# Optimization experiments

Hardware: AMD Instinct MI355X
Metric: run time of the kernel (lower is better)

Reference implementation:

```python
import jax, jax.numpy as jnp
import numpy as np
from jax import lax

BN_EPS = 1e-5


def conv(x, w, b, pad):
    # x: NCHW, w: OIHW
    y = lax.conv_general_dilated(x, w, (1, 1), [(pad, pad), (pad, pad)],
                                 dimension_numbers=('NCHW', 'OIHW', 'NCHW'))
    return y + b[None, :, None, None]


def conv_t(x, w, b):
    # ConvTranspose2d, stride=1, padding=0, kernel 3. w is torch layout [in, out, kh, kw].
    # Equivalent to a regular conv with spatially flipped kernel, in/out swapped, full padding (kh-1=2).
    wf = jnp.transpose(jnp.flip(w, (2, 3)), (1, 0, 2, 3))  # [out, in, kh, kw]
    y = lax.conv_general_dilated(x, wf, (1, 1), [(2, 2), (2, 2)],
                                 dimension_numbers=('NCHW', 'OIHW', 'NCHW'))
    return y + b[None, :, None, None]


def bn(x, g, be):
    # BatchNorm2d, training-mode batch stats (biased variance), gamma/beta learnable.
    mu = x.mean((0, 2, 3), keepdims=True)
    var = x.var((0, 2, 3), keepdims=True)
    xn = (x - mu) * lax.rsqrt(var + BN_EPS)
    return g[None, :, None, None] * xn + be[None, :, None, None]


def setup_inputs() -> dict:
    key = jax.random.key(0)
    ks = jax.random.split(key, 20)
    B, C, H, W = 16, 64, 44, 44
    P = H * W  # 1936

    def kaiming(k, shape, fan_out):
        return jax.random.normal(k, shape, jnp.float32) * np.sqrt(2.0 / fan_out)

    inp = {
        'depth': jax.random.normal(ks[0], (B, C, H, W), jnp.float32),
        'rgb': jax.random.normal(ks[1], (B, C, H, W), jnp.float32),
        # h_c / h_f conv layers: Conv2d(128, 64, 3, padding=1)
        'w_hc': kaiming(ks[2], (64, 128, 3, 3), 64 * 9), 'b_hc': jnp.zeros((64,), jnp.float32),
        'w_hf': kaiming(ks[3], (64, 128, 3, 3), 64 * 9), 'b_hf': jnp.zeros((64,), jnp.float32),
        # spatial_pool_agr
        'w_s1': kaiming(ks[4], (32, P, 3, 3), 32 * 9), 'bs1': jnp.zeros((32,), jnp.float32),
        'g1': jnp.ones((32,), jnp.float32), 'be1': jnp.zeros((32,), jnp.float32),
        'w_s2': kaiming(ks[5], (32, 32, 3, 3), 32 * 9), 'bs2': jnp.zeros((32,), jnp.float32),
        'g2': jnp.ones((32,), jnp.float32), 'be2': jnp.zeros((32,), jnp.float32),
        # ConvTranspose2d weights in torch layout [in, out, kh, kw]
        'w_d1': kaiming(ks[6], (32, 32, 3, 3), 32 * 9), 'bd1': jnp.zeros((32,), jnp.float32),
        'g3': jnp.ones((32,), jnp.float32), 'be3': jnp.zeros((32,), jnp.float32),
        'w_d2': kaiming(ks[7], (32, 1, 3, 3), 1 * 9), 'bd2': jnp.zeros((1,), jnp.float32),
        # channel_pool_ag: Linear(64, 16), Linear(16, 64)
        'w_l1': kaiming(ks[8], (16, 64), 16), 'bl1': jnp.zeros((16,), jnp.float32),
        'w_l2': kaiming(ks[9], (64, 16), 64), 'bl2': jnp.zeros((64,), jnp.float32),
    }
    return inp


def reference(depth, rgb, w_hc, b_hc, w_hf, b_hf,
              w_s1, bs1, g1, be1, w_s2, bs2, g2, be2,
              w_d1, bd1, g3, be3, w_d2, bd2,
              w_l1, bl1, w_l2, bl2):
    B, C, H, W = depth.shape
    # fused rgb+depth conv
    h_c = jnp.concatenate([rgb, depth], axis=1)          # [B, 2C, H, W]
    h_c_conv = jax.nn.relu(conv(h_c, w_hc, b_hc, 1))      # [B, 64, H, W]

    # per-pixel correlation: grouped 1x1 conv == batched matmul
    # pixel_corr[b, p, y, x] = sum_c rgb[b, c, y, x] * depth[b, c, p]
    pixel_corr = jnp.einsum('bchw,bcp->bphw', rgb, depth.reshape(B, C, H * W))

    x = jax.nn.relu(bn(conv(pixel_corr, w_s1, bs1, 0), g1, be1))  # 44 -> 42
    x = jax.nn.relu(bn(conv(x, w_s2, bs2, 0), g2, be2))           # 42 -> 40
    x = jax.nn.relu(bn(conv_t(x, w_d1, bd1), g3, be3))            # 40 -> 42
    spatial_att = jax.nn.sigmoid(conv_t(x, w_d2, bd2))            # [B, 1, 44, 44]

    # per-channel correlation: grouped full-extent conv == elementwise dot per (b, c)
    depth_corr = jnp.sum(rgb * depth, axis=(2, 3))                # [B, C]
    # MaxPool2d(1)/AvgPool2d(1) are identities -> both branches are identical
    def mlp(v):
        return jax.nn.relu(v @ w_l1.T + bl1) @ w_l2.T + bl2
    m = mlp(depth_corr)
    channel_att = jax.nn.sigmoid(m + m)[:, :, None, None]         # [B, C, 1, 1]

    h_att = jnp.concatenate([h_c_conv * spatial_att, h_c_conv * channel_att], axis=1)
    return jax.nn.relu(conv(h_att, w_hf, b_hf, 1))                # [B, 64, 44, 44]
```

## Files before the change

kernel.cpp:

```cpp
#include <hip/hip_runtime.h>
#include <math.h>

#define P_ 1936
#define EPS_ 1e-5f

typedef __attribute__((ext_vector_type(8))) short bf16x8;
typedef __attribute__((ext_vector_type(4))) float f32x4;
typedef __attribute__((ext_vector_type(4))) ushort u16x4;

__device__ __forceinline__ ushort f2bf(float f) {
    union { float f; unsigned u; } v; v.f = f;
    unsigned u = v.u;
    return (ushort)((u + 0x7FFFu + ((u >> 16) & 1u)) >> 16);
}
__device__ __forceinline__ float bf2f(ushort h) {
    union { unsigned u; float f; } v; v.u = (unsigned)h << 16;
    return v.f;
}

__device__ __forceinline__ void bn_coef(const float* stats, const float* g,
                                        const float* be, int ch, float inv_n,
                                        float& sc, float& sh) {
    float sum = stats[ch*2], sq = stats[ch*2+1];
    float mu = sum * inv_n;
    float var = sq * inv_n - mu*mu;
    float r = rsqrtf(var + EPS_);
    sc = g[ch] * r;
    sh = be[ch] - mu * sc;
}

__global__ __launch_bounds__(256) void k_setup(const float* __restrict__ whc,
                                               const float* __restrict__ whf,
                                               const float* __restrict__ ws2,
                                               const float* __restrict__ wd1,
                                               const float* __restrict__ ws1,
                                               const float* __restrict__ rgb,
                                               const float* __restrict__ depth,
                                               ushort* __restrict__ wpck,
                                               ushort* __restrict__ a2,
                                               ushort* __restrict__ a3,
                                               ushort* __restrict__ apck1,
                                               ushort* __restrict__ xp,
                                               ushort* __restrict__ depthb,
                                               float* __restrict__ dcor,
                                               float* __restrict__ stats) {
    __shared__ float r8[8];
    const int bx = blockIdx.x, t = threadIdx.x;
    if (bx < 2808) {
        if (bx == 0 && t < 192) stats[t] = 0.f;
        int idx = bx * 256 + t;
        if (idx < 147456) {
            const float* src = (idx < 73728) ? whc : whf;
            int j = (idx < 73728) ? idx : idx - 73728;
            int kk = j / 8192, rem = j - kk * 8192;
            int o = rem >> 7, c = rem & 127;
            wpck[(idx < 73728 ? 0 : 73728) + (kk * 64 + o) * 128 + c] =
                f2bf(src[(size_t)(o * 128 + c) * 9 + kk]);
        } else if (idx < 156672) {
            int j = idx - 147456;
            int kk = j >> 10, rem = j & 1023, o = rem >> 5, c = rem & 31;
            a2[j] = f2bf(ws2[((size_t)o*32 + c)*9 + kk]);
            a3[j] = f2bf(wd1[((size_t)c*32 + o)*9 + (8 - kk)]);
        } else if (idx < 718848) {
            int j = idx - 156672;
            int m = j / 1952, p = j - m*1952;
            int o = m / 9, kk = m - o*9;
            apck1[j] = (p < P_) ? f2bf(ws1[((size_t)o*P_ + p)*9 + kk]) : (ushort)0;
        }
        return;
    }
    const int j = bx - 2808;
    const int g8 = j & 7, b = j >> 3;
    const int c0 = g8 * 8;
    const float* rsrc = rgb   + ((size_t)b*64 + c0)*P_;
    const float* dsrc = depth + ((size_t)b*64 + c0)*P_;
    ushort* xr = xp + ((size_t)(b*16 + g8))*2300*8;
    ushort* xd = xp + ((size_t)(b*16 + 8 + g8))*2300*8;
    if (t < 8) r8[t] = 0.f;
    __syncthreads();
    float dc[8];
    #pragma unroll
    for (int e = 0; e < 8; ++e) dc[e] = 0.f;

    for (int pos = t; pos < 2300; pos += 256) {
        int y1 = pos / 50, x1 = pos - y1*50;
        uint4 vr = {0u,0u,0u,0u}, vd = {0u,0u,0u,0u};
        if (y1 >= 1 && y1 <= 44 && x1 >= 1 && x1 <= 44) {
            int p = (y1-1)*44 + (x1-1);
            ushort hr[8], hd[8];
            #pragma unroll
            for (int e = 0; e < 8; ++e) {
                float fr = rsrc[(size_t)e*P_ + p];
                float fd = dsrc[(size_t)e*P_ + p];
                dc[e] = fmaf(fr, fd, dc[e]);
                hr[e] = f2bf(fr); hd[e] = f2bf(fd);
            }
            vr.x = hr[0] | ((unsigned)hr[1] << 16); vr.y = hr[2] | ((unsigned)hr[3] << 16);
            vr.z = hr[4] | ((unsigned)hr[5] << 16); vr.w = hr[6] | ((unsigned)hr[7] << 16);
            vd.x = hd[0] | ((unsigned)hd[1] << 16); vd.y = hd[2] | ((unsigned)hd[3] << 16);
            vd.z = hd[4] | ((unsigned)hd[5] << 16); vd.w = hd[6] | ((unsigned)hd[7] << 16);
        }
        *(uint4*)(xr + (size_t)pos*8) = vr;
        *(uint4*)(xd + (size_t)pos*8) = vd;
    }
    for (int idx = t; idx < 8*488; idx += 256) {
        int e = idx / 488, jj = idx - e*488;
        u16x4 h = {0,0,0,0};
        if (jj < 484) {
            float4 f4 = *(const float4*)(dsrc + (size_t)e*P_ + jj*4);
            h[0] = f2bf(f4.x); h[1] = f2bf(f4.y); h[2] = f2bf(f4.z); h[3] = f2bf(f4.w);
        }
        *(u16x4*)(depthb + ((size_t)(b*64 + c0 + e))*1952 + jj*4) = h;
    }
    #pragma unroll
    for (int e = 0; e < 8; ++e) {
        float v = dc[e];
        #pragma unroll
        for (int off = 32; off > 0; off >>= 1) v += __shfl_down(v, off, 64);
        if ((t & 63) == 0) atomicAdd(&r8[e], v);
    }
    __syncthreads();
    if (t < 8) dcor[b*64 + c0 + t] = r8[t];
}

__global__ __launch_bounds__(256) void k_hcconv(const ushort* __restrict__ xp,
                                                const ushort* __restrict__ wt,
                                                const float* __restrict__ bias,
                                                ushort* __restrict__ hcp) {
    __shared__ ushort lds[9616];
    const int rt = blockIdx.x, og = blockIdx.y, b = blockIdx.z, t = threadIdx.x;
    const int w = t >> 6, lane = t & 63, lr = lane & 15, lg = lane >> 4;
    const int r0 = rt * 4;
    f32x4 acc[2][3];
    #pragma unroll
    for (int mf = 0; mf < 2; ++mf)
        #pragma unroll
        for (int nf = 0; nf < 3; ++nf)
            acc[mf][nf] = (f32x4){0.f, 0.f, 0.f, 0.f};

    for (int s = 0; s < 4; ++s) {
        __syncthreads();
        const ushort* gsrc = xp + ((size_t)(b*16 + s*4))*2300*8;
        for (int u = t; u < 1200; u += 256) {
            int cg = u / 300, rem = u - cg*300;
            int rr = rem / 50, xx = rem - rr*50;
            uint4 v = *(const uint4*)(gsrc + (((size_t)cg*46 + (r0+rr))*50 + xx)*8);
            *(uint4*)(lds + (size_t)u*8) = v;
        }
        __syncthreads();
        const int abase = s*32 + lg*8;
        #pragma unroll
        for (int kk = 0; kk < 9; ++kk) {
            bf16x8 af[2];
            #pragma unroll
            for (int mf = 0; mf < 2; ++mf)
                af[mf] = *(const bf16x8*)(wt + (size_t)(kk*64 + og*32 + mf*16 + lr)*128 + abase);
            const int ky = kk / 3, kx = kk - ky*3;
            #pragma unroll
            for (int nf = 0; nf < 3; ++nf) {
                bf16x8 bf = *(const bf16x8*)&lds[((lg*6 + (w + ky))*50 + (nf*16 + lr + kx))*8];
                #pragma unroll
                for (int mf = 0; mf < 2; ++mf)
                    acc[mf][nf] = __builtin_amdgcn_mfma_f32_16x16x32_bf16(af[mf], bf, acc[mf][nf], 0, 0, 0);
            }
        }
    }
    const int y = r0 + w;
    #pragma unroll
    for (int nf = 0; nf < 3; ++nf) {
        int x = nf*16 + lr;
        if (x < 44) {
            #pragma unroll
            for (int mf = 0; mf < 2; ++mf) {
                u16x4 pk;
                #pragma unroll
                for (int i = 0; i < 4; ++i) {
                    int ol = mf*16 + lg*4 + i;
                    pk[i] = f2bf(fmaxf(acc[mf][nf][i] + bias[og*32 + ol], 0.f));
                }
                int g = og*4 + mf*2 + (lg >> 1);
                *(u16x4*)(hcp + (((size_t)(b*8 + g)*46 + (y+1))*50 + (x+1))*8 + (lg&1)*4) = pk;
            }
        }
    }
}

__global__ __launch_bounds__(256) void k_final(const ushort* __restrict__ hcp,
                                               const float* __restrict__ satt,
                                               const float* __restrict__ catt,
                                               const ushort* __restrict__ wt,
                                               const float* __restrict__ bias,
                                               float* __restrict__ out) {
    __shared__ ushort lds[9616];
    __shared__ float catv[64];
    const int rt = blockIdx.x, og = blockIdx.y, b = blockIdx.z, t = threadIdx.x;
    const int w = t >> 6, lane = t & 63, lr = lane & 15, lg = lane >> 4;
    const int r0 = rt * 4;
    if (t < 64) catv[t] = catt[b*64 + t];
    f32x4 acc[2][3];
    #pragma unroll
    for (int mf = 0; mf < 2; ++mf)
        #pragma unroll
        for (int nf = 0; nf < 3; ++nf)
            acc[mf][nf] = (f32x4){0.f, 0.f, 0.f, 0.f};

    for (int s = 0; s < 4; ++s) {
        __syncthreads();
        for (int u = t; u < 1200; u += 256) {
            int cg = u / 300, rem = u - cg*300;
            int rr = rem / 50, xx = rem - rr*50;
            int g = s*4 + cg;
            int y1 = r0 + rr;
            uint4 v = {0u,0u,0u,0u};
            if (y1 >= 1 && y1 <= 44 && xx >= 1 && xx <= 44) {
                int gs = (g < 8) ? g : (g - 8);
                uint4 raw = *(const uint4*)(hcp + (((size_t)(b*8 + gs)*46 + y1)*50 + xx)*8);
                unsigned arr[4] = {raw.x, raw.y, raw.z, raw.w};
                ushort h[8];
                if (g < 8) {
                    float att = satt[(size_t)b*P_ + (y1-1)*44 + (xx-1)];
                    #pragma unroll
                    for (int e = 0; e < 8; ++e) {
                        ushort hv = (e & 1) ? (ushort)(arr[e>>1] >> 16) : (ushort)(arr[e>>1] & 0xffffu);
                        h[e] = f2bf(bf2f(hv) * att);
                    }
                } else {
                    #pragma unroll
                    for (int e = 0; e < 8; ++e) {
                        ushort hv = (e & 1) ? (ushort)(arr[e>>1] >> 16) : (ushort)(arr[e>>1] & 0xffffu);
                        h[e] = f2bf(bf2f(hv) * catv[(g-8)*8 + e]);
                    }
                }
                v.x = h[0] | ((unsigned)h[1] << 16);
                v.y = h[2] | ((unsigned)h[3] << 16);
                v.z = h[4] | ((unsigned)h[5] << 16);
                v.w = h[6] | ((unsigned)h[7] << 16);
            }
            *(uint4*)(lds + (size_t)u*8) = v;
        }
        __syncthreads();
        const int abase = s*32 + lg*8;
        #pragma unroll
        for (int kk = 0; kk < 9; ++kk) {
            bf16x8 af[2];
            #pragma unroll
            for (int mf = 0; mf < 2; ++mf)
                af[mf] = *(const bf16x8*)(wt + (size_t)(kk*64 + og*32 + mf*16 + lr)*128 + abase);
            const int ky = kk / 3, kx = kk - ky*3;
            #pragma unroll
            for (int nf = 0; nf < 3; ++nf) {
                bf16x8 bf = *(const bf16x8*)&lds[((lg*6 + (w + ky))*50 + (nf*16 + lr + kx))*8];
                #pragma unroll
                for (int mf = 0; mf < 2; ++mf)
                    acc[mf][nf] = __builtin_amdgcn_mfma_f32_16x16x32_bf16(af[mf], bf, acc[mf][nf], 0, 0, 0);
            }
        }
    }
    const int y = r0 + w;
    #pragma unroll
    for (int nf = 0; nf < 3; ++nf) {
        int x = nf*16 + lr;
        if (x < 44) {
            #pragma unroll
            for (int mf = 0; mf < 2; ++mf) {
                #pragma unroll
                for (int i = 0; i < 4; ++i) {
                    int o = og*32 + mf*16 + lg*4 + i;
                    out[(((size_t)b*64 + o)*44 + y)*44 + x] = fmaxf(acc[mf][nf][i] + bias[o], 0.f);
                }
            }
        }
    }
}

__global__ __launch_bounds__(256) void k_Umfma(const ushort* __restrict__ apck1,
                                               const ushort* __restrict__ depthb,
                                               ushort* __restrict__ upck,
                                               const float* __restrict__ dcorr,
                                               const float* __restrict__ wl1,
                                               const float* __restrict__ bl1,
                                               const float* __restrict__ wl2,
                                               const float* __restrict__ bl2,
                                               float* __restrict__ catt) {
    const int mt = blockIdx.x, b = blockIdx.y, t = threadIdx.x;
    if (mt == 18) {
        __shared__ float dc[64], h[16];
        if (t < 64) dc[t] = dcorr[b*64 + t];
        __syncthreads();
        if (t < 16) {
            float a = bl1[t];
            #pragma unroll 8
            for (int c = 0; c < 64; ++c) a = fmaf(dc[c], wl1[t*64 + c], a);
            h[t] = fmaxf(a, 0.f);
        }
        __syncthreads();
        if (t < 64) {
            float m = bl2[t];
            #pragma unroll
            for (int jj = 0; jj < 16; ++jj) m = fmaf(h[jj], wl2[t*16 + jj], m);
            catt[b*64 + t] = 1.f / (1.f + expf(-2.f*m));
        }
        return;
    }
    const int nt = t >> 6, lane = t & 63, lr = lane & 15, lg = lane >> 4;
    f32x4 acc = (f32x4){0.f, 0.f, 0.f, 0.f};
    const ushort* ap = apck1 + (size_t)(mt*16 + lr)*1952 + lg*8;
    const ushort* bp = depthb + ((size_t)(b*64) + nt*16 + lr)*1952 + lg*8;
    #pragma unroll 4
    for (int ks = 0; ks < 61; ++ks) {
        bf16x8 af = *(const bf16x8*)(ap + ks*32);
        bf16x8 bf = *(const bf16x8*)(bp + ks*32);
        acc = __builtin_amdgcn_mfma_f32_16x16x32_bf16(af, bf, acc, 0, 0, 0);
    }
    #pragma unroll
    for (int i = 0; i < 4; ++i) {
        int m = mt*16 + lg*4 + i;
        int o = m / 9, kk = m - o*9;
        upck[((size_t)(b*9 + kk)*32 + o)*64 + nt*16 + lr] = f2bf(acc[i]);
    }
}

__global__ __launch_bounds__(256) void k_conv1_mfma(const ushort* __restrict__ xp,
                                                    const ushort* __restrict__ upck,
                                                    const float* __restrict__ bs1,
                                                    ushort* __restrict__ z1p,
                                                    float* __restrict__ stats) {
    __shared__ ushort lds[8*6*50*8 + 32];
    __shared__ float ssum[32], ssq[32];
    const int rt = blockIdx.x, b = blockIdx.y, t = threadIdx.x;
    const int w = t >> 6, lane = t & 63, lr = lane & 15, lg = lane >> 4;
    const int r0 = rt * 4;
    if (t < 32) { ssum[t] = 0.f; ssq[t] = 0.f; }
    f32x4 acc[2][3];
    #pragma unroll
    for (int mf = 0; mf < 2; ++mf)
        #pragma unroll
        for (int nf = 0; nf < 3; ++nf)
            acc[mf][nf] = (f32x4){0.f, 0.f, 0.f, 0.f};

    const ushort* gsrc = xp + (size_t)b*16*2300*8;
    for (int u = t; u < 2400; u += 256) {
        int cg = u / 300, rem = u - cg*300;
        int rr = rem / 50, xx = rem - rr*50;
        int y1 = min(r0 + 1 + rr, 45);
        *(uint4*)(lds + (size_t)u*8) = *(const uint4*)(gsrc + (((size_t)cg*46 + y1)*50 + xx)*8);
    }
    __syncthreads();
    #pragma unroll
    for (int s = 0; s < 2; ++s) {
        #pragma unroll
        for (int kk = 0; kk < 9; ++kk) {
            bf16x8 af[2];
            #pragma unroll
            for (int mf = 0; mf < 2; ++mf)
                af[mf] = *(const bf16x8*)(upck + ((size_t)(b*9 + kk)*32 + mf*16 + lr)*64 + s*32 + lg*8);
            const int ky = kk / 3, kx = kk - ky*3;
            #pragma unroll
            for (int nf = 0; nf < 3; ++nf) {
                bf16x8 bv = *(const bf16x8*)&lds[(((s*4 + lg)*6 + (w + ky))*50 + (nf*16 + lr + kx + 1))*8];
                #pragma unroll
                for (int mf = 0; mf < 2; ++mf)
                    acc[mf][nf] = __builtin_amdgcn_mfma_f32_16x16x32_bf16(af[mf], bv, acc[mf][nf], 0, 0, 0);
            }
        }
    }
    const int y = r0 + w;
    const int cb = lg*4;
    if (y < 42) {
        float ls[2][4], lq[2][4], br[2][4];
        #pragma unroll
        for (int mf = 0; mf < 2; ++mf)
            #pragma unroll
            for (int i = 0; i < 4; ++i) {
                ls[mf][i] = 0.f; lq[mf][i] = 0.f;
                br[mf][i] = bs1[mf*16 + cb + i];
            }
        #pragma unroll
        for (int nf = 0; nf < 3; ++nf) {
            int x = nf*16 + lr;
            bool xv = (x < 42);
            #pragma unroll
            for (int mf = 0; mf < 2; ++mf) {
                u16x4 pk;
                #pragma unroll
                for (int i = 0; i < 4; ++i) {
                    float v = acc[mf][nf][i] + br[mf][i];
                    if (xv) { ls[mf][i] += v; lq[mf][i] = fmaf(v, v, lq[mf][i]); }
                    pk[i] = f2bf(v);
                }
                if (xv) {
                    int cg1 = mf*2 + (lg >> 1);
                    *(u16x4*)(z1p + ((((size_t)b*4 + cg1)*42 + y)*48 + x)*8 + (lg&1)*4) = pk;
                }
            }
        }
        #pragma unroll
        for (int mf = 0; mf < 2; ++mf)
            #pragma unroll
            for (int i = 0; i < 4; ++i) {
                float s0 = ls[mf][i], q0 = lq[mf][i];
                #pragma unroll
                for (int m = 1; m < 16; m <<= 1) { s0 += __shfl_xor(s0, m, 64); q0 += __shfl_xor(q0, m, 64); }
                if (lr == 0) { atomicAdd(&ssum[mf*16 + cb + i], s0); atomicAdd(&ssq[mf*16 + cb + i], q0); }
            }
    }
    __syncthreads();
    if (t < 32) { atomicAdd(&stats[t*2], ssum[t]); atomicAdd(&stats[t*2+1], ssq[t]); }
}

__global__ __launch_bounds__(256) void k_conv2_mfma(const ushort* __restrict__ z1p,
                                                    const ushort* __restrict__ apck,
                                                    const float* __restrict__ bs2,
                                                    const float* __restrict__ g1,
                                                    const float* __restrict__ be1,
                                                    const float* __restrict__ statsIn,
                                                    ushort* __restrict__ z2p,
                                                    float* __restrict__ statsOut) {
    __shared__ ushort lds[4*6*48*8 + 32];
    __shared__ float sc[32], sh[32], ssum[32], ssq[32];
    const int rt = blockIdx.x, b = blockIdx.y, t = threadIdx.x;
    const int w = t >> 6, lane = t & 63, lr = lane & 15, lg = lane >> 4;
    const int r0 = rt * 4;
    if (t < 32) {
        bn_coef(statsIn, g1, be1, t, 1.f/28224.f, sc[t], sh[t]);
        ssum[t] = 0.f; ssq[t] = 0.f;
    }
    __syncthreads();
    f32x4 acc[2][3];
    #pragma unroll
    for (int mf = 0; mf < 2; ++mf)
        #pragma unroll
        for (int nf = 0; nf < 3; ++nf)
            acc[mf][nf] = (f32x4){0.f, 0.f, 0.f, 0.f};

    for (int u = t; u < 1152; u += 256) {
        int cg = u / 288, rem = u - cg*288;
        int rr = rem / 48, xx = rem - rr*48;
        uint4 raw = *(const uint4*)(z1p + ((((size_t)b*4 + cg)*42 + (r0 + rr))*48 + xx)*8);
        unsigned arr[4] = {raw.x, raw.y, raw.z, raw.w};
        ushort h[8];
        #pragma unroll
        for (int e = 0; e < 8; ++e) {
            ushort hv = (e & 1) ? (ushort)(arr[e>>1] >> 16) : (ushort)(arr[e>>1] & 0xffffu);
            float f = fmaxf(fmaf(bf2f(hv), sc[cg*8 + e], sh[cg*8 + e]), 0.f);
            h[e] = f2bf(f);
        }
        uint4 v;
        v.x = h[0] | ((unsigned)h[1] << 16);
        v.y = h[2] | ((unsigned)h[3] << 16);
        v.z = h[4] | ((unsigned)h[5] << 16);
        v.w = h[6] | ((unsigned)h[7] << 16);
        *(uint4*)(lds + (size_t)u*8) = v;
    }
    __syncthreads();
    #pragma unroll
    for (int kk = 0; kk < 9; ++kk) {
        bf16x8 af[2];
        #pragma unroll
        for (int mf = 0; mf < 2; ++mf)
            af[mf] = *(const bf16x8*)(apck + (size_t)(kk*32 + mf*16 + lr)*32 + lg*8);
        const int ky = kk / 3, kx = kk - ky*3;
        #pragma unroll
        for (int nf = 0; nf < 3; ++nf) {
            bf16x8 bv = *(const bf16x8*)&lds[((lg*6 + (w + ky))*48 + (nf*16 + lr + kx))*8];
            #pragma unroll
            for (int mf = 0; mf < 2; ++mf)
                acc[mf][nf] = __builtin_amdgcn_mfma_f32_16x16x32_bf16(af[mf], bv, acc[mf][nf], 0, 0, 0);
        }
    }
    const int y = r0 + w;
    const int cb = lg*4;
    {
        float ls[2][4], lq[2][4], br[2][4];
        #pragma unroll
        for (int mf = 0; mf < 2; ++mf)
            #pragma unroll
            for (int i = 0; i < 4; ++i) {
                ls[mf][i] = 0.f; lq[mf][i] = 0.f;
                br[mf][i] = bs2[mf*16 + cb + i];
            }
        #pragma unroll
        for (int nf = 0; nf < 3; ++nf) {
            int x = nf*16 + lr;
            bool xv = (x < 40);
            #pragma unroll
            for (int mf = 0; mf < 2; ++mf) {
                u16x4 pk;
                #pragma unroll
                for (int i = 0; i < 4; ++i) {
                    float v = acc[mf][nf][i] + br[mf][i];
                    if (xv) { ls[mf][i] += v; lq[mf][i] = fmaf(v, v, lq[mf][i]); }
                    pk[i] = f2bf(v);
                }
                if (xv) {
                    int cg1 = mf*2 + (lg >> 1);
                    *(u16x4*)(z2p + ((((size_t)b*4 + cg1)*46 + (y+2))*48 + (x+2))*8 + (lg&1)*4) = pk;
                }
            }
        }
        #pragma unroll
        for (int mf = 0; mf < 2; ++mf)
            #pragma unroll
            for (int i = 0; i < 4; ++i) {
                float s0 = ls[mf][i], q0 = lq[mf][i];
                #pragma unroll
                for (int m = 1; m < 16; m <<= 1) { s0 += __shfl_xor(s0, m, 64); q0 += __shfl_xor(q0, m, 64); }
                if (lr == 0) { atomicAdd(&ssum[mf*16 + cb + i], s0); atomicAdd(&ssq[mf*16 + cb + i], q0); }
            }
    }
    __syncthreads();
    if (t < 32) { atomicAdd(&statsOut[t*2], ssum[t]); atomicAdd(&statsOut[t*2+1], ssq[t]); }
}

__global__ __launch_bounds__(256) void k_dconv1_mfma(const ushort* __restrict__ z2p,
                                                     const ushort* __restrict__ apck,
                                                     const float* __restrict__ bd1,
                                                     const float* __restrict__ g2,
                                                     const float* __restrict__ be2,
                                                     const float* __restrict__ statsIn,
                                                     ushort* __restrict__ z3p,
                                                     float* __restrict__ statsOut) {
    __shared__ ushort lds[4*6*48*8 + 32];
    __shared__ float sc[32], sh[32], ssum[32], ssq[32];
    const int rt = blockIdx.x, b = blockIdx.y, t = threadIdx.x;
    const int w = t >> 6, lane = t & 63, lr = lane & 15, lg = lane >> 4;
    const int r0 = rt * 4;
    if (t < 32) {
        bn_coef(statsIn, g2, be2, t, 1.f/25600.f, sc[t], sh[t]);
        ssum[t] = 0.f; ssq[t] = 0.f;
    }
    __syncthreads();
    f32x4 acc[2][3];
    #pragma unroll
    for (int mf = 0; mf < 2; ++mf)
        #pragma unroll
        for (int nf = 0; nf < 3; ++nf)
            acc[mf][nf] = (f32x4){0.f, 0.f, 0.f, 0.f};

    for (int u = t; u < 1152; u += 256) {
        int cg = u / 288, rem = u - cg*288;
        int rr = rem / 48, xx = rem - rr*48;
        int row = r0 + rr;
        uint4 v = {0u,0u,0u,0u};
        if (row >= 2 && row <= 41 && xx >= 2 && xx <= 41) {
            uint4 raw = *(const uint4*)(z2p + ((((size_t)b*4 + cg)*46 + row)*48 + xx)*8);
            unsigned arr[4] = {raw.x, raw.y, raw.z, raw.w};
            ushort h[8];
            #pragma unroll
            for (int e = 0; e < 8; ++e) {
                ushort hv = (e & 1) ? (ushort)(arr[e>>1] >> 16) : (ushort)(arr[e>>1] & 0xffffu);
                float f = fmaxf(fmaf(bf2f(hv), sc[cg*8 + e], sh[cg*8 + e]), 0.f);
                h[e] = f2bf(f);
            }
            v.x = h[0] | ((unsigned)h[1] << 16);
            v.y = h[2] | ((unsigned)h[3] << 16);
            v.z = h[4] | ((unsigned)h[5] << 16);
            v.w = h[6] | ((unsigned)h[7] << 16);
        }
        *(uint4*)(lds + (size_t)u*8) = v;
    }
    __syncthreads();
    #pragma unroll
    for (int kk = 0; kk < 9; ++kk) {
        bf16x8 af[2];
        #pragma unroll
        for (int mf = 0; mf < 2; ++mf)
            af[mf] = *(const bf16x8*)(apck + (size_t)(kk*32 + mf*16 + lr)*32 + lg*8);
        const int ky = kk / 3, kx = kk - ky*3;
        #pragma unroll
        for (int nf = 0; nf < 3; ++nf) {
            bf16x8 bv = *(const bf16x8*)&lds[((lg*6 + (w + ky))*48 + (nf*16 + lr + kx))*8];
            #pragma unroll
            for (int mf = 0; mf < 2; ++mf)
                acc[mf][nf] = __builtin_amdgcn_mfma_f32_16x16x32_bf16(af[mf], bv, acc[mf][nf], 0, 0, 0);
        }
    }
    const int y = r0 + w;
    const int cb = lg*4;
    if (y < 42) {
        float ls[2][4], lq[2][4], br[2][4];
        #pragma unroll
        for (int mf = 0; mf < 2; ++mf)
            #pragma unroll
            for (int i = 0; i < 4; ++i) {
                ls[mf][i] = 0.f; lq[mf][i] = 0.f;
                br[mf][i] = bd1[mf*16 + cb + i];
            }
        #pragma unroll
        for (int nf = 0; nf < 3; ++nf) {
            int x = nf*16 + lr;
            bool xv = (x < 42);
            #pragma unroll
            for (int mf = 0; mf < 2; ++mf) {
                u16x4 pk;
                #pragma unroll
                for (int i = 0; i < 4; ++i) {
                    float v = acc[mf][nf][i] + br[mf][i];
                    if (xv) { ls[mf][i] += v; lq[mf][i] = fmaf(v, v, lq[mf][i]); }
                    pk[i] = f2bf(v);
                }
                if (xv) {
                    int cg1 = mf*2 + (lg >> 1);
                    *(u16x4*)(z3p + ((((size_t)b*4 + cg1)*46 + (y+2))*48 + (x+2))*8 + (lg&1)*4) = pk;
                }
            }
        }
        #pragma unroll
        for (int mf = 0; mf < 2; ++mf)
            #pragma unroll
            for (int i = 0; i < 4; ++i) {
                float s0 = ls[mf][i], q0 = lq[mf][i];
                #pragma unroll
                for (int m = 1; m < 16; m <<= 1) { s0 += __shfl_xor(s0, m, 64); q0 += __shfl_xor(q0, m, 64); }
                if (lr == 0) { atomicAdd(&ssum[mf*16 + cb + i], s0); atomicAdd(&ssq[mf*16 + cb + i], q0); }
            }
    }
    __syncthreads();
    if (t < 32) { atomicAdd(&statsOut[t*2], ssum[t]); atomicAdd(&statsOut[t*2+1], ssq[t]); }
}

__global__ __launch_bounds__(256) void k_dconv2(const ushort* __restrict__ z3p,
                                                const float* __restrict__ wd2,
                                                const float* __restrict__ bd2,
                                                const float* __restrict__ g3,
                                                const float* __restrict__ be3,
                                                const float* __restrict__ stats,
                                                float* __restrict__ satt) {
    __shared__ float sc[32], sh[32], wf[32][9];
    const int b = blockIdx.y, t = threadIdx.x;
    if (t < 32) bn_coef(stats, g3, be3, t, 1.f/28224.f, sc[t], sh[t]);
    for (int u = t; u < 288; u += 256) {
        int c = u / 9, k = u - c*9;
        wf[c][k] = wd2[c*9 + 8 - k];
    }
    __syncthreads();
    const int pix = blockIdx.x * 256 + t;
    if (pix >= P_) return;
    const int y = pix / 44, x = pix - y*44;
    float acc = bd2[0];
    #pragma unroll
    for (int kk = 0; kk < 9; ++kk) {
        int ky = kk / 3, kx = kk - ky*3;
        int ry = y + ky, rx = x + kx;
        if (ry < 2 || ry > 43 || rx < 2 || rx > 43) continue;
        #pragma unroll
        for (int cg = 0; cg < 4; ++cg) {
            uint4 raw = *(const uint4*)(z3p + ((((size_t)b*4 + cg)*46 + ry)*48 + rx)*8);
            unsigned arr[4] = {raw.x, raw.y, raw.z, raw.w};
            #pragma unroll
            for (int e = 0; e < 8; ++e) {
                ushort hv = (e & 1) ? (ushort)(arr[e>>1] >> 16) : (ushort)(arr[e>>1] & 0xffffu);
                float f = fmaxf(fmaf(bf2f(hv), sc[cg*8 + e], sh[cg*8 + e]), 0.f);
                acc = fmaf(f, wf[cg*8 + e][kk], acc);
            }
        }
    }
    satt[(size_t)b*P_ + pix] = 1.f / (1.f + expf(-acc));
}

extern "C" void kernel_launch(void* const* d_in, const int* in_sizes, int n_in,
                              void* d_out, int out_size, void* d_ws, size_t ws_size,
                              hipStream_t stream) {
    const float* depth = (const float*)d_in[0];
    const float* rgb   = (const float*)d_in[1];
    const float* w_hc  = (const float*)d_in[2];
    const float* b_hc  = (const float*)d_in[3];
    const float* w_hf  = (const float*)d_in[4];
    const float* b_hf  = (const float*)d_in[5];
    const float* w_s1  = (const float*)d_in[6];
    const float* bs1   = (const float*)d_in[7];
    const float* g1    = (const float*)d_in[8];
    const float* be1   = (const float*)d_in[9];
    const float* w_s2  = (const float*)d_in[10];
    const float* bs2   = (const float*)d_in[11];
    const float* g2    = (const float*)d_in[12];
    const float* be2   = (const float*)d_in[13];
    const float* w_d1  = (const float*)d_in[14];
    const float* bd1   = (const float*)d_in[15];
    const float* g3    = (const float*)d_in[16];
    const float* be3   = (const float*)d_in[17];
    const float* w_d2  = (const float*)d_in[18];
    const float* bd2   = (const float*)d_in[19];
    const float* w_l1  = (const float*)d_in[20];
    const float* bl1   = (const float*)d_in[21];
    const float* w_l2  = (const float*)d_in[22];
    const float* bl2   = (const float*)d_in[23];

    float* out = (float*)d_out;
    float* ws  = (float*)d_ws;

    float* satt  = ws;
    float* catt  = satt + 30976;
    float* dcor  = catt + 1024;
    float* stats = dcor + 1024;
    ushort* hcp    = (ushort*)(stats + 192);
    ushort* wpck   = hcp    + 2355200;
    ushort* apck2  = wpck   + 147456;
    ushort* apck3  = apck2  + 9216;
    ushort* apck1  = apck3  + 9216;
    ushort* depthb = apck1  + 562176;
    ushort* upck   = depthb + 1998848;
    ushort* z1p    = upck   + 294912;
    ushort* z2p    = z1p    + 1032192;
    ushort* z3p    = z2p    + 1130496;
    ushort* xpck   = z3p    + 1130496;

    k_setup<<<2936, 256, 0, stream>>>(w_hc, w_hf, w_s2, w_d1, w_s1, rgb, depth,
                                      wpck, apck2, apck3, apck1, xpck, depthb, dcor, stats);

    k_hcconv<<<dim3(11,2,16), 256, 0, stream>>>(xpck, wpck, b_hc, hcp);
    k_Umfma<<<dim3(19,16), 256, 0, stream>>>(apck1, depthb, upck,
                                             dcor, w_l1, bl1, w_l2, bl2, catt);

    k_conv1_mfma<<<dim3(11,16), 256, 0, stream>>>(xpck, upck, bs1, z1p, stats);
    k_conv2_mfma<<<dim3(10,16), 256, 0, stream>>>(z1p, apck2, bs2, g1, be1, stats, z2p, stats + 64);
    k_dconv1_mfma<<<dim3(11,16), 256, 0, stream>>>(z2p, apck3, bd1, g2, be2, stats + 64, z3p, stats + 128);
    k_dconv2<<<dim3(8,16), 256, 0, stream>>>(z3p, w_d2, bd2, g3, be3, stats + 128, satt);

    k_final<<<dim3(11,2,16), 256, 0, stream>>>(hcp, satt, catt, wpck + 73728, b_hf, out);
}
```

Measured before the change: 156.4 us.

## Split setup input-packing blocks 4x and merge hc-conv with U-matmul kernel

The rgb/depth packing part of the setup kernel is split into four position chunks per (batch, channel-group), so it runs as 512 blocks instead of 128. The per-channel dot products are written as four partials that the MLP block sums. The hc conv and the U matmul/MLP kernels are merged into one launch of 656 blocks, which removes a launch and lets the two independent kernels fill the GPU together. The cost is more, smaller blocks and an extra partial-sum buffer.

```diff
diff --git a/kernel.cpp b/kernel.cpp
--- a/kernel.cpp
+++ b/kernel.cpp
@@ -42,7 +42,7 @@
                                                ushort* __restrict__ apck1,
                                                ushort* __restrict__ xp,
                                                ushort* __restrict__ depthb,
-                                               float* __restrict__ dcor,
+                                               float* __restrict__ dcor_part,
                                                float* __restrict__ stats) {
     __shared__ float r8[8];
     const int bx = blockIdx.x, t = threadIdx.x;
@@ -70,7 +70,7 @@
         return;
     }
     const int j = bx - 2808;
-    const int g8 = j & 7, b = j >> 3;
+    const int g8 = j & 7, b = (j >> 3) & 15, q = j >> 7;
     const int c0 = g8 * 8;
     const float* rsrc = rgb   + ((size_t)b*64 + c0)*P_;
     const float* dsrc = depth + ((size_t)b*64 + c0)*P_;
@@ -82,7 +82,8 @@
     #pragma unroll
     for (int e = 0; e < 8; ++e) dc[e] = 0.f;
 
-    for (int pos = t; pos < 2300; pos += 256) {
+    const int pbase = q * 575;
+    for (int pos = pbase + t; pos < pbase + 575; pos += 256) {
         int y1 = pos / 50, x1 = pos - y1*50;
         uint4 vr = {0u,0u,0u,0u}, vd = {0u,0u,0u,0u};
         if (y1 >= 1 && y1 <= 44 && x1 >= 1 && x1 <= 44) {
@@ -103,7 +104,7 @@
         *(uint4*)(xr + (size_t)pos*8) = vr;
         *(uint4*)(xd + (size_t)pos*8) = vd;
     }
-    for (int idx = t; idx < 8*488; idx += 256) {
+    for (int idx = q*976 + t; idx < q*976 + 976; idx += 256) {
         int e = idx / 488, jj = idx - e*488;
         u16x4 h = {0,0,0,0};
         if (jj < 484) {
@@ -120,17 +121,135 @@
         if ((t & 63) == 0) atomicAdd(&r8[e], v);
     }
     __syncthreads();
-    if (t < 8) dcor[b*64 + c0 + t] = r8[t];
-}
-
-__global__ __launch_bounds__(256) void k_hcconv(const ushort* __restrict__ xp,
-                                                const ushort* __restrict__ wt,
-                                                const float* __restrict__ bias,
-                                                ushort* __restrict__ hcp) {
+    if (t < 8) dcor_part[q*1024 + b*64 + c0 + t] = r8[t];
+}
+
+__global__ __launch_bounds__(256) void k_front(const ushort* __restrict__ xp,
+                                               const ushort* __restrict__ wt,
+                                               const float* __restrict__ bhc,
+                                               ushort* __restrict__ hcp,
+                                               const ushort* __restrict__ apck1,
+                                               const ushort* __restrict__ depthb,
+                                               ushort* __restrict__ upck,
+                                               const float* __restrict__ dcor_part,
+                                               const float* __restrict__ wl1,
+                                               const float* __restrict__ bl1,
+                                               const float* __restrict__ wl2,
+                                               const float* __restrict__ bl2,
+                                               float* __restrict__ catt) {
     __shared__ ushort lds[9616];
-    const int rt = blockIdx.x, og = blockIdx.y, b = blockIdx.z, t = threadIdx.x;
+    __shared__ float mlpb[80];
+    const int bx = blockIdx.x, t = threadIdx.x;
+    if (bx < 352) {
+        const int rt = bx % 11, og = (bx / 11) & 1, b = bx / 22;
+        const int w = t >> 6, lane = t & 63, lr = lane & 15, lg = lane >> 4;
+        const int r0 = rt * 4;
+        f32x4 acc[2][3];
+        #pragma unroll
+        for (int mf = 0; mf < 2; ++mf)
+            #pragma unroll
+            for (int nf = 0; nf < 3; ++nf)
+                acc[mf][nf] = (f32x4){0.f, 0.f, 0.f, 0.f};
+
+        for (int s = 0; s < 4; ++s) {
+            __syncthreads();
+            const ushort* gsrc = xp + ((size_t)(b*16 + s*4))*2300*8;
+            for (int u = t; u < 1200; u += 256) {
+                int cg = u / 300, rem = u - cg*300;
+                int rr = rem / 50, xx = rem - rr*50;
+                uint4 v = *(const uint4*)(gsrc + (((size_t)cg*46 + (r0+rr))*50 + xx)*8);
+                *(uint4*)(lds + (size_t)u*8) = v;
+            }
+            __syncthreads();
+            const int abase = s*32 + lg*8;
+            #pragma unroll
+            for (int kk = 0; kk < 9; ++kk) {
+                bf16x8 af[2];
+                #pragma unroll
+                for (int mf = 0; mf < 2; ++mf)
+                    af[mf] = *(const bf16x8*)(wt + (size_t)(kk*64 + og*32 + mf*16 + lr)*128 + abase);
+                const int ky = kk / 3, kx = kk - ky*3;
+                #pragma unroll
+                for (int nf = 0; nf < 3; ++nf) {
+                    bf16x8 bf = *(const bf16x8*)&lds[((lg*6 + (w + ky))*50 + (nf*16 + lr + kx))*8];
+                    #pragma unroll
+                    for (int mf = 0; mf < 2; ++mf)
+                        acc[mf][nf] = __builtin_amdgcn_mfma_f32_16x16x32_bf16(af[mf], bf, acc[mf][nf], 0, 0, 0);
+                }
+            }
+        }
+        const int y = r0 + w;
+        #pragma unroll
+        for (int nf = 0; nf < 3; ++nf) {
+            int x = nf*16 + lr;
+            if (x < 44) {
+                #pragma unroll
+                for (int mf = 0; mf < 2; ++mf) {
+                    u16x4 pk;
+                    #pragma unroll
+                    for (int i = 0; i < 4; ++i) {
+                        int ol = og*32 + mf*16 + lg*4 + i;
+                        pk[i] = f2bf(fmaxf(acc[mf][nf][i] + bhc[ol], 0.f));
+                    }
+                    int g = og*4 + mf*2 + (lg >> 1);
+                    *(u16x4*)(hcp + (((size_t)(b*8 + g)*46 + (y+1))*50 + (x+1))*8 + (lg&1)*4) = pk;
+                }
+            }
+        }
+        return;
+    }
+    const int j = bx - 352;
+    const int mt = j % 19, b = j / 19;
+    if (mt == 18) {
+        float* dcs = mlpb;
+        float* h   = mlpb + 64;
+        if (t < 64) dcs[t] = dcor_part[b*64 + t] + dcor_part[1024 + b*64 + t]
+                           + dcor_part[2048 + b*64 + t] + dcor_part[3072 + b*64 + t];
+        __syncthreads();
+        if (t < 16) {
+            float a = bl1[t];
+            #pragma unroll 8
+            for (int c = 0; c < 64; ++c) a = fmaf(dcs[c], wl1[t*64 + c], a);
+            h[t] = fmaxf(a, 0.f);
+        }
+        __syncthreads();
+        if (t < 64) {
+            float m = bl2[t];
+            #pragma unroll
+            for (int jj = 0; jj < 16; ++jj) m = fmaf(h[jj], wl2[t*16 + jj], m);
+            catt[b*64 + t] = 1.f / (1.f + expf(-2.f*m));
+        }
+        return;
+    }
+    const int nt = t >> 6, lane = t & 63, lr = lane & 15, lg = lane >> 4;
+    f32x4 acc = (f32x4){0.f, 0.f, 0.f, 0.f};
+    const ushort* ap = apck1 + (size_t)(mt*16 + lr)*1952 + lg*8;
+    const ushort* bp = depthb + ((size_t)(b*64) + nt*16 + lr)*1952 + lg*8;
+    #pragma unroll 4
+    for (int ks = 0; ks < 61; ++ks) {
+        bf16x8 af = *(const bf16x8*)(ap + ks*32);
+        bf16x8 bf = *(const bf16x8*)(bp + ks*32);
+        acc = __builtin_amdgcn_mfma_f32_16x16x32_bf16(af, bf, acc, 0, 0, 0);
+    }
+    #pragma unroll
+    for (int i = 0; i < 4; ++i) {
+        int m = mt*16 + lg*4 + i;
+        int o = m / 9, kk = m - o*9;
+        upck[((size_t)(b*9 + kk)*32 + o)*64 + nt*16 + lr] = f2bf(acc[i]);
+    }
+}
+
+__global__ __launch_bounds__(256) void k_conv1_mfma(const ushort* __restrict__ xp,
+                                                    const ushort* __restrict__ upck,
+                                                    const float* __restrict__ bs1,
+                                                    ushort* __restrict__ z1p,
+                                                    float* __restrict__ stats) {
+    __shared__ ushort lds[8*6*50*8 + 32];
+    __shared__ float ssum[32], ssq[32];
+    const int rt = blockIdx.x, b = blockIdx.y, t = threadIdx.x;
     const int w = t >> 6, lane = t & 63, lr = lane & 15, lg = lane >> 4;
     const int r0 = rt * 4;
+    if (t < 32) { ssum[t] = 0.f; ssq[t] = 0.f; }
     f32x4 acc[2][3];
     #pragma unroll
     for (int mf = 0; mf < 2; ++mf)
@@ -138,51 +257,324 @@
         for (int nf = 0; nf < 3; ++nf)
             acc[mf][nf] = (f32x4){0.f, 0.f, 0.f, 0.f};
 
-    for (int s = 0; s < 4; ++s) {
-        __syncthreads();
-        const ushort* gsrc = xp + ((size_t)(b*16 + s*4))*2300*8;
-        for (int u = t; u < 1200; u += 256) {
-            int cg = u / 300, rem = u - cg*300;
-            int rr = rem / 50, xx = rem - rr*50;
-            uint4 v = *(const uint4*)(gsrc + (((size_t)cg*46 + (r0+rr))*50 + xx)*8);
-            *(uint4*)(lds + (size_t)u*8) = v;
-        }
-        __syncthreads();
-        const int abase = s*32 + lg*8;
+    const ushort* gsrc = xp + (size_t)b*16*2300*8;
+    for (int u = t; u < 2400; u += 256) {
+        int cg = u / 300, rem = u - cg*300;
+        int rr = rem / 50, xx = rem - rr*50;
+        int y1 = min(r0 + 1 + rr, 45);
+        *(uint4*)(lds + (size_t)u*8) = *(const uint4*)(gsrc + (((size_t)cg*46 + y1)*50 + xx)*8);
+    }
+    __syncthreads();
+    #pragma unroll
+    for (int s = 0; s < 2; ++s) {
         #pragma unroll
         for (int kk = 0; kk < 9; ++kk) {
             bf16x8 af[2];
             #pragma unroll
             for (int mf = 0; mf < 2; ++mf)
-                af[mf] = *(const bf16x8*)(wt + (size_t)(kk*64 + og*32 + mf*16 + lr)*128 + abase);
+                af[mf] = *(const bf16x8*)(upck + ((size_t)(b*9 + kk)*32 + mf*16 + lr)*64 + s*32 + lg*8);
             const int ky = kk / 3, kx = kk - ky*3;
             #pragma unroll
             for (int nf = 0; nf < 3; ++nf) {
-                bf16x8 bf = *(const bf16x8*)&lds[((lg*6 + (w + ky))*50 + (nf*16 + lr + kx))*8];
+                bf16x8 bv = *(const bf16x8*)&lds[(((s*4 + lg)*6 + (w + ky))*50 + (nf*16 + lr + kx + 1))*8];
                 #pragma unroll
                 for (int mf = 0; mf < 2; ++mf)
-                    acc[mf][nf] = __builtin_amdgcn_mfma_f32_16x16x32_bf16(af[mf], bf, acc[mf][nf], 0, 0, 0);
+                    acc[mf][nf] = __builtin_amdgcn_mfma_f32_16x16x32_bf16(af[mf], bv, acc[mf][nf], 0, 0, 0);
             }
         }
     }
     const int y = r0 + w;
-    #pragma unroll
-    for (int nf = 0; nf < 3; ++nf) {
-        int x = nf*16 + lr;
-        if (x < 44) {
+    const int cb = lg*4;
+    if (y < 42) {
+        float ls[2][4], lq[2][4], br[2][4];
+        #pragma unroll
+        for (int mf = 0; mf < 2; ++mf)
+            #pragma unroll
+            for (int i = 0; i < 4; ++i) {
+                ls[mf][i] = 0.f; lq[mf][i] = 0.f;
+                br[mf][i] = bs1[mf*16 + cb + i];
+            }
+        #pragma unroll
+        for (int nf = 0; nf < 3; ++nf) {
+            int x = nf*16 + lr;
+            bool xv = (x < 42);
             #pragma unroll
             for (int mf = 0; mf < 2; ++mf) {
                 u16x4 pk;
                 #pragma unroll
                 for (int i = 0; i < 4; ++i) {
-                    int ol = mf*16 + lg*4 + i;
-                    pk[i] = f2bf(fmaxf(acc[mf][nf][i] + bias[og*32 + ol], 0.f));
-                }
-                int g = og*4 + mf*2 + (lg >> 1);
-                *(u16x4*)(hcp + (((size_t)(b*8 + g)*46 + (y+1))*50 + (x+1))*8 + (lg&1)*4) = pk;
-            }
-        }
-    }
+                    float v = acc[mf][nf][i] + br[mf][i];
+                    if (xv) { ls[mf][i] += v; lq[mf][i] = fmaf(v, v, lq[mf][i]); }
+                    pk[i] = f2bf(v);
+                }
+                if (xv) {
+                    int cg1 = mf*2 + (lg >> 1);
+                    *(u16x4*)(z1p + ((((size_t)b*4 + cg1)*42 + y)*48 + x)*8 + (lg&1)*4) = pk;
+                }
+            }
+        }
+        #pragma unroll
+        for (int mf = 0; mf < 2; ++mf)
+            #pragma unroll
+            for (int i = 0; i < 4; ++i) {
+                float s0 = ls[mf][i], q0 = lq[mf][i];
+                #pragma unroll
+                for (int m = 1; m < 16; m <<= 1) { s0 += __shfl_xor(s0, m, 64); q0 += __shfl_xor(q0, m, 64); }
+                if (lr == 0) { atomicAdd(&ssum[mf*16 + cb + i], s0); atomicAdd(&ssq[mf*16 + cb + i], q0); }
+            }
+    }
+    __syncthreads();
+    if (t < 32) { atomicAdd(&stats[t*2], ssum[t]); atomicAdd(&stats[t*2+1], ssq[t]); }
+}
+
+__global__ __launch_bounds__(256) void k_conv2_mfma(const ushort* __restrict__ z1p,
+                                                    const ushort* __restrict__ apck,
+                                                    const float* __restrict__ bs2,
+                                                    const float* __restrict__ g1,
+                                                    const float* __restrict__ be1,
+                                                    const float* __restrict__ statsIn,
+                                                    ushort* __restrict__ z2p,
+                                                    float* __restrict__ statsOut) {
+    __shared__ ushort lds[4*6*48*8 + 32];
+    __shared__ float sc[32], sh[32], ssum[32], ssq[32];
+    const int rt = blockIdx.x, b = blockIdx.y, t = threadIdx.x;
+    const int w = t >> 6, lane = t & 63, lr = lane & 15, lg = lane >> 4;
+    const int r0 = rt * 4;
+    if (t < 32) {
+        bn_coef(statsIn, g1, be1, t, 1.f/28224.f, sc[t], sh[t]);
+        ssum[t] = 0.f; ssq[t] = 0.f;
+    }
+    __syncthreads();
+    f32x4 acc[2][3];
+    #pragma unroll
+    for (int mf = 0; mf < 2; ++mf)
+        #pragma unroll
+        for (int nf = 0; nf < 3; ++nf)
+            acc[mf][nf] = (f32x4){0.f, 0.f, 0.f, 0.f};
+
+    for (int u = t; u < 1152; u += 256) {
+        int cg = u / 288, rem = u - cg*288;
+        int rr = rem / 48, xx = rem - rr*48;
+        uint4 raw = *(const uint4*)(z1p + ((((size_t)b*4 + cg)*42 + (r0 + rr))*48 + xx)*8);
+        unsigned arr[4] = {raw.x, raw.y, raw.z, raw.w};
+        ushort h[8];
+        #pragma unroll
+        for (int e = 0; e < 8; ++e) {
+            ushort hv = (e & 1) ? (ushort)(arr[e>>1] >> 16) : (ushort)(arr[e>>1] & 0xffffu);
+            float f = fmaxf(fmaf(bf2f(hv), sc[cg*8 + e], sh[cg*8 + e]), 0.f);
+            h[e] = f2bf(f);
+        }
+        uint4 v;
+        v.x = h[0] | ((unsigned)h[1] << 16);
+        v.y = h[2] | ((unsigned)h[3] << 16);
+        v.z = h[4] | ((unsigned)h[5] << 16);
+        v.w = h[6] | ((unsigned)h[7] << 16);
+        *(uint4*)(lds + (size_t)u*8) = v;
+    }
+    __syncthreads();
+    #pragma unroll
+    for (int kk = 0; kk < 9; ++kk) {
+        bf16x8 af[2];
+        #pragma unroll
+        for (int mf = 0; mf < 2; ++mf)
+            af[mf] = *(const bf16x8*)(apck + (size_t)(kk*32 + mf*16 + lr)*32 + lg*8);
+        const int ky = kk / 3, kx = kk - ky*3;
+        #pragma unroll
+        for (int nf = 0; nf < 3; ++nf) {
+            bf16x8 bv = *(const bf16x8*)&lds[((lg*6 + (w + ky))*48 + (nf*16 + lr + kx))*8];
+            #pragma unroll
+            for (int mf = 0; mf < 2; ++mf)
+                acc[mf][nf] = __builtin_amdgcn_mfma_f32_16x16x32_bf16(af[mf], bv, acc[mf][nf], 0, 0, 0);
+        }
+    }
+    const int y = r0 + w;
+    const int cb = lg*4;
+    {
+        float ls[2][4], lq[2][4], br[2][4];
+        #pragma unroll
+        for (int mf = 0; mf < 2; ++mf)
+            #pragma unroll
+            for (int i = 0; i < 4; ++i) {
+                ls[mf][i] = 0.f; lq[mf][i] = 0.f;
+                br[mf][i] = bs2[mf*16 + cb + i];
+            }
+        #pragma unroll
+        for (int nf = 0; nf < 3; ++nf) {
+            int x = nf*16 + lr;
+            bool xv = (x < 40);
+            #pragma unroll
+            for (int mf = 0; mf < 2; ++mf) {
+                u16x4 pk;
+                #pragma unroll
+                for (int i = 0; i < 4; ++i) {
+                    float v = acc[mf][nf][i] + br[mf][i];
+                    if (xv) { ls[mf][i] += v; lq[mf][i] = fmaf(v, v, lq[mf][i]); }
+                    pk[i] = f2bf(v);
+                }
+                if (xv) {
+                    int cg1 = mf*2 + (lg >> 1);
+                    *(u16x4*)(z2p + ((((size_t)b*4 + cg1)*46 + (y+2))*48 + (x+2))*8 + (lg&1)*4) = pk;
+                }
+            }
+        }
+        #pragma unroll
+        for (int mf = 0; mf < 2; ++mf)
+            #pragma unroll
+            for (int i = 0; i < 4; ++i) {
+                float s0 = ls[mf][i], q0 = lq[mf][i];
+                #pragma unroll
+                for (int m = 1; m < 16; m <<= 1) { s0 += __shfl_xor(s0, m, 64); q0 += __shfl_xor(q0, m, 64); }
+                if (lr == 0) { atomicAdd(&ssum[mf*16 + cb + i], s0); atomicAdd(&ssq[mf*16 + cb + i], q0); }
+            }
+    }
+    __syncthreads();
+    if (t < 32) { atomicAdd(&statsOut[t*2], ssum[t]); atomicAdd(&statsOut[t*2+1], ssq[t]); }
+}
+
+__global__ __launch_bounds__(256) void k_dconv1_mfma(const ushort* __restrict__ z2p,
+                                                     const ushort* __restrict__ apck,
+                                                     const float* __restrict__ bd1,
+                                                     const float* __restrict__ g2,
+                                                     const float* __restrict__ be2,
+                                                     const float* __restrict__ statsIn,
+                                                     ushort* __restrict__ z3p,
+                                                     float* __restrict__ statsOut) {
+    __shared__ ushort lds[4*6*48*8 + 32];
+    __shared__ float sc[32], sh[32], ssum[32], ssq[32];
+    const int rt = blockIdx.x, b = blockIdx.y, t = threadIdx.x;
+    const int w = t >> 6, lane = t & 63, lr = lane & 15, lg = lane >> 4;
+    const int r0 = rt * 4;
+    if (t < 32) {
+        bn_coef(statsIn, g2, be2, t, 1.f/25600.f, sc[t], sh[t]);
+        ssum[t] = 0.f; ssq[t] = 0.f;
+    }
+    __syncthreads();
+    f32x4 acc[2][3];
+    #pragma unroll
+    for (int mf = 0; mf < 2; ++mf)
+        #pragma unroll
+        for (int nf = 0; nf < 3; ++nf)
+            acc[mf][nf] = (f32x4){0.f, 0.f, 0.f, 0.f};
+
+    for (int u = t; u < 1152; u += 256) {
+        int cg = u / 288, rem = u - cg*288;
+        int rr = rem / 48, xx = rem - rr*48;
+        int row = r0 + rr;
+        uint4 v = {0u,0u,0u,0u};
+        if (row >= 2 && row <= 41 && xx >= 2 && xx <= 41) {
+            uint4 raw = *(const uint4*)(z2p + ((((size_t)b*4 + cg)*46 + row)*48 + xx)*8);
+            unsigned arr[4] = {raw.x, raw.y, raw.z, raw.w};
+            ushort h[8];
+            #pragma unroll
+            for (int e = 0; e < 8; ++e) {
+                ushort hv = (e & 1) ? (ushort)(arr[e>>1] >> 16) : (ushort)(arr[e>>1] & 0xffffu);
+                float f = fmaxf(fmaf(bf2f(hv), sc[cg*8 + e], sh[cg*8 + e]), 0.f);
+                h[e] = f2bf(f);
+            }
+            v.x = h[0] | ((unsigned)h[1] << 16);
+            v.y = h[2] | ((unsigned)h[3] << 16);
+            v.z = h[4] | ((unsigned)h[5] << 16);
+            v.w = h[6] | ((unsigned)h[7] << 16);
+        }
+        *(uint4*)(lds + (size_t)u*8) = v;
+    }
+    __syncthreads();
+    #pragma unroll
+    for (int kk = 0; kk < 9; ++kk) {
+        bf16x8 af[2];
+        #pragma unroll
+        for (int mf = 0; mf < 2; ++mf)
+            af[mf] = *(const bf16x8*)(apck + (size_t)(kk*32 + mf*16 + lr)*32 + lg*8);
+        const int ky = kk / 3, kx = kk - ky*3;
+        #pragma unroll
+        for (int nf = 0; nf < 3; ++nf) {
+            bf16x8 bv = *(const bf16x8*)&lds[((lg*6 + (w + ky))*48 + (nf*16 + lr + kx))*8];
+            #pragma unroll
+            for (int mf = 0; mf < 2; ++mf)
+                acc[mf][nf] = __builtin_amdgcn_mfma_f32_16x16x32_bf16(af[mf], bv, acc[mf][nf], 0, 0, 0);
+        }
+    }
+    const int y = r0 + w;
+    const int cb = lg*4;
+    if (y < 42) {
+        float ls[2][4], lq[2][4], br[2][4];
+        #pragma unroll
+        for (int mf = 0; mf < 2; ++mf)
+            #pragma unroll
+            for (int i = 0; i < 4; ++i) {
+                ls[mf][i] = 0.f; lq[mf][i] = 0.f;
+                br[mf][i] = bd1[mf*16 + cb + i];
+            }
+        #pragma unroll
+        for (int nf = 0; nf < 3; ++nf) {
+            int x = nf*16 + lr;
+            bool xv = (x < 42);
+            #pragma unroll
+            for (int mf = 0; mf < 2; ++mf) {
+                u16x4 pk;
+                #pragma unroll
+                for (int i = 0; i < 4; ++i) {
+                    float v = acc[mf][nf][i] + br[mf][i];
+                    if (xv) { ls[mf][i] += v; lq[mf][i] = fmaf(v, v, lq[mf][i]); }
+                    pk[i] = f2bf(v);
+                }
+                if (xv) {
+                    int cg1 = mf*2 + (lg >> 1);
+                    *(u16x4*)(z3p + ((((size_t)b*4 + cg1)*46 + (y+2))*48 + (x+2))*8 + (lg&1)*4) = pk;
+                }
+            }
+        }
+        #pragma unroll
+        for (int mf = 0; mf < 2; ++mf)
+            #pragma unroll
+            for (int i = 0; i < 4; ++i) {
+                float s0 = ls[mf][i], q0 = lq[mf][i];
+                #pragma unroll
+                for (int m = 1; m < 16; m <<= 1) { s0 += __shfl_xor(s0, m, 64); q0 += __shfl_xor(q0, m, 64); }
+                if (lr == 0) { atomicAdd(&ssum[mf*16 + cb + i], s0); atomicAdd(&ssq[mf*16 + cb + i], q0); }
+            }
+    }
+    __syncthreads();
+    if (t < 32) { atomicAdd(&statsOut[t*2], ssum[t]); atomicAdd(&statsOut[t*2+1], ssq[t]); }
+}
+
+__global__ __launch_bounds__(256) void k_dconv2(const ushort* __restrict__ z3p,
+                                                const float* __restrict__ wd2,
+                                                const float* __restrict__ bd2,
+                                                const float* __restrict__ g3,
+                                                const float* __restrict__ be3,
+                                                const float* __restrict__ stats,
+                                                float* __restrict__ satt) {
+    __shared__ float sc[32], sh[32], wf[32][9];
+    const int b = blockIdx.y, t = threadIdx.x;
+    if (t < 32) bn_coef(stats, g3, be3, t, 1.f/28224.f, sc[t], sh[t]);
+    for (int u = t; u < 288; u += 256) {
+        int c = u / 9, k = u - c*9;
+        wf[c][k] = wd2[c*9 + 8 - k];
+    }
+    __syncthreads();
+    const int pix = blockIdx.x * 256 + t;
+    if (pix >= P_) return;
+    const int y = pix / 44, x = pix - y*44;
+    float acc = bd2[0];
+    #pragma unroll
+    for (int kk = 0; kk < 9; ++kk) {
+        int ky = kk / 3, kx = kk - ky*3;
+        int ry = y + ky, rx = x + kx;
+        if (ry < 2 || ry > 43 || rx < 2 || rx > 43) continue;
+        #pragma unroll
+        for (int cg = 0; cg < 4; ++cg) {
+            uint4 raw = *(const uint4*)(z3p + ((((size_t)b*4 + cg)*46 + ry)*48 + rx)*8);
+            unsigned arr[4] = {raw.x, raw.y, raw.z, raw.w};
+            #pragma unroll
+            for (int e = 0; e < 8; ++e) {
+                ushort hv = (e & 1) ? (ushort)(arr[e>>1] >> 16) : (ushort)(arr[e>>1] & 0xffffu);
+                float f = fmaxf(fmaf(bf2f(hv), sc[cg*8 + e], sh[cg*8 + e]), 0.f);
+                acc = fmaf(f, wf[cg*8 + e][kk], acc);
+            }
+        }
+    }
+    satt[(size_t)b*P_ + pix] = 1.f / (1.f + expf(-acc));
 }
 
 __global__ __launch_bounds__(256) void k_final(const ushort* __restrict__ hcp,
@@ -271,391 +663,6 @@
             }
         }
     }
-}
-
-__global__ __launch_bounds__(256) void k_Umfma(const ushort* __restrict__ apck1,
-                                               const ushort* __restrict__ depthb,
-                                               ushort* __restrict__ upck,
-                                               const float* __restrict__ dcorr,
-                                               const float* __restrict__ wl1,
-                                               const float* __restrict__ bl1,
-                                               const float* __restrict__ wl2,
-                                               const float* __restrict__ bl2,
-                                               float* __restrict__ catt) {
-    const int mt = blockIdx.x, b = blockIdx.y, t = threadIdx.x;
-    if (mt == 18) {
-        __shared__ float dc[64], h[16];
-        if (t < 64) dc[t] = dcorr[b*64 + t];
-        __syncthreads();
-        if (t < 16) {
-            float a = bl1[t];
-            #pragma unroll 8
-            for (int c = 0; c < 64; ++c) a = fmaf(dc[c], wl1[t*64 + c], a);
-            h[t] = fmaxf(a, 0.f);
-        }
-        __syncthreads();
-        if (t < 64) {
-            float m = bl2[t];
-            #pragma unroll
-            for (int jj = 0; jj < 16; ++jj) m = fmaf(h[jj], wl2[t*16 + jj], m);
-            catt[b*64 + t] = 1.f / (1.f + expf(-2.f*m));
-        }
-        return;
-    }
-    const int nt = t >> 6, lane = t & 63, lr = lane & 15, lg = lane >> 4;
-    f32x4 acc = (f32x4){0.f, 0.f, 0.f, 0.f};
-    const ushort* ap = apck1 + (size_t)(mt*16 + lr)*1952 + lg*8;
-    const ushort* bp = depthb + ((size_t)(b*64) + nt*16 + lr)*1952 + lg*8;
-    #pragma unroll 4
-    for (int ks = 0; ks < 61; ++ks) {
-        bf16x8 af = *(const bf16x8*)(ap + ks*32);
-        bf16x8 bf = *(const bf16x8*)(bp + ks*32);
-        acc = __builtin_amdgcn_mfma_f32_16x16x32_bf16(af, bf, acc, 0, 0, 0);
-    }
-    #pragma unroll
-    for (int i = 0; i < 4; ++i) {
-        int m = mt*16 + lg*4 + i;
-        int o = m / 9, kk = m - o*9;
-        upck[((size_t)(b*9 + kk)*32 + o)*64 + nt*16 + lr] = f2bf(acc[i]);
-    }
-}
-
-__global__ __launch_bounds__(256) void k_conv1_mfma(const ushort* __restrict__ xp,
-                                                    const ushort* __restrict__ upck,
-                                                    const float* __restrict__ bs1,
-                                                    ushort* __restrict__ z1p,
-                                                    float* __restrict__ stats) {
-    __shared__ ushort lds[8*6*50*8 + 32];
-    __shared__ float ssum[32], ssq[32];
-    const int rt = blockIdx.x, b = blockIdx.y, t = threadIdx.x;
-    const int w = t >> 6, lane = t & 63, lr = lane & 15, lg = lane >> 4;
-    const int r0 = rt * 4;
-    if (t < 32) { ssum[t] = 0.f; ssq[t] = 0.f; }
-    f32x4 acc[2][3];
-    #pragma unroll
-    for (int mf = 0; mf < 2; ++mf)
-        #pragma unroll
-        for (int nf = 0; nf < 3; ++nf)
-            acc[mf][nf] = (f32x4){0.f, 0.f, 0.f, 0.f};
-
-    const ushort* gsrc = xp + (size_t)b*16*2300*8;
-    for (int u = t; u < 2400; u += 256) {
-        int cg = u / 300, rem = u - cg*300;
-        int rr = rem / 50, xx = rem - rr*50;
-        int y1 = min(r0 + 1 + rr, 45);
-        *(uint4*)(lds + (size_t)u*8) = *(const uint4*)(gsrc + (((size_t)cg*46 + y1)*50 + xx)*8);
-    }
-    __syncthreads();
-    #pragma unroll
-    for (int s = 0; s < 2; ++s) {
-        #pragma unroll
-        for (int kk = 0; kk < 9; ++kk) {
-            bf16x8 af[2];
-            #pragma unroll
-            for (int mf = 0; mf < 2; ++mf)
-                af[mf] = *(const bf16x8*)(upck + ((size_t)(b*9 + kk)*32 + mf*16 + lr)*64 + s*32 + lg*8);
-            const int ky = kk / 3, kx = kk - ky*3;
-            #pragma unroll
-            for (int nf = 0; nf < 3; ++nf) {
-                bf16x8 bv = *(const bf16x8*)&lds[(((s*4 + lg)*6 + (w + ky))*50 + (nf*16 + lr + kx + 1))*8];
-                #pragma unroll
-                for (int mf = 0; mf < 2; ++mf)
-                    acc[mf][nf] = __builtin_amdgcn_mfma_f32_16x16x32_bf16(af[mf], bv, acc[mf][nf], 0, 0, 0);
-            }
-        }
-    }
-    const int y = r0 + w;
-    const int cb = lg*4;
-    if (y < 42) {
-        float ls[2][4], lq[2][4], br[2][4];
-        #pragma unroll
-        for (int mf = 0; mf < 2; ++mf)
-            #pragma unroll
-            for (int i = 0; i < 4; ++i) {
-                ls[mf][i] = 0.f; lq[mf][i] = 0.f;
-                br[mf][i] = bs1[mf*16 + cb + i];
-            }
-        #pragma unroll
-        for (int nf = 0; nf < 3; ++nf) {
-            int x = nf*16 + lr;
-            bool xv = (x < 42);
-            #pragma unroll
-            for (int mf = 0; mf < 2; ++mf) {
-                u16x4 pk;
-                #pragma unroll
-                for (int i = 0; i < 4; ++i) {
-                    float v = acc[mf][nf][i] + br[mf][i];
-                    if (xv) { ls[mf][i] += v; lq[mf][i] = fmaf(v, v, lq[mf][i]); }
-                    pk[i] = f2bf(v);
-                }
-                if (xv) {
-                    int cg1 = mf*2 + (lg >> 1);
-                    *(u16x4*)(z1p + ((((size_t)b*4 + cg1)*42 + y)*48 + x)*8 + (lg&1)*4) = pk;
-                }
-            }
-        }
-        #pragma unroll
-        for (int mf = 0; mf < 2; ++mf)
-            #pragma unroll
-            for (int i = 0; i < 4; ++i) {
-                float s0 = ls[mf][i], q0 = lq[mf][i];
-                #pragma unroll
-                for (int m = 1; m < 16; m <<= 1) { s0 += __shfl_xor(s0, m, 64); q0 += __shfl_xor(q0, m, 64); }
-                if (lr == 0) { atomicAdd(&ssum[mf*16 + cb + i], s0); atomicAdd(&ssq[mf*16 + cb + i], q0); }
-            }
-    }
-    __syncthreads();
-    if (t < 32) { atomicAdd(&stats[t*2], ssum[t]); atomicAdd(&stats[t*2+1], ssq[t]); }
-}
-
-__global__ __launch_bounds__(256) void k_conv2_mfma(const ushort* __restrict__ z1p,
-                                                    const ushort* __restrict__ apck,
-                                                    const float* __restrict__ bs2,
-                                                    const float* __restrict__ g1,
-                                                    const float* __restrict__ be1,
-                                                    const float* __restrict__ statsIn,
-                                                    ushort* __restrict__ z2p,
-                                                    float* __restrict__ statsOut) {
-    __shared__ ushort lds[4*6*48*8 + 32];
-    __shared__ float sc[32], sh[32], ssum[32], ssq[32];
-    const int rt = blockIdx.x, b = blockIdx.y, t = threadIdx.x;
-    const int w = t >> 6, lane = t & 63, lr = lane & 15, lg = lane >> 4;
-    const int r0 = rt * 4;
-    if (t < 32) {
-        bn_coef(statsIn, g1, be1, t, 1.f/28224.f, sc[t], sh[t]);
-        ssum[t] = 0.f; ssq[t] = 0.f;
-    }
-    __syncthreads();
-    f32x4 acc[2][3];
-    #pragma unroll
-    for (int mf = 0; mf < 2; ++mf)
-        #pragma unroll
-        for (int nf = 0; nf < 3; ++nf)
-            acc[mf][nf] = (f32x4){0.f, 0.f, 0.f, 0.f};
-
-    for (int u = t; u < 1152; u += 256) {
-        int cg = u / 288, rem = u - cg*288;
-        int rr = rem / 48, xx = rem - rr*48;
-        uint4 raw = *(const uint4*)(z1p + ((((size_t)b*4 + cg)*42 + (r0 + rr))*48 + xx)*8);
-        unsigned arr[4] = {raw.x, raw.y, raw.z, raw.w};
-        ushort h[8];
-        #pragma unroll
-        for (int e = 0; e < 8; ++e) {
-            ushort hv = (e & 1) ? (ushort)(arr[e>>1] >> 16) : (ushort)(arr[e>>1] & 0xffffu);
-            float f = fmaxf(fmaf(bf2f(hv), sc[cg*8 + e], sh[cg*8 + e]), 0.f);
-            h[e] = f2bf(f);
-        }
-        uint4 v;
-        v.x = h[0] | ((unsigned)h[1] << 16);
-        v.y = h[2] | ((unsigned)h[3] << 16);
-        v.z = h[4] | ((unsigned)h[5] << 16);
-        v.w = h[6] | ((unsigned)h[7] << 16);
-        *(uint4*)(lds + (size_t)u*8) = v;
-    }
-    __syncthreads();
-    #pragma unroll
-    for (int kk = 0; kk < 9; ++kk) {
-        bf16x8 af[2];
-        #pragma unroll
-        for (int mf = 0; mf < 2; ++mf)
-            af[mf] = *(const bf16x8*)(apck + (size_t)(kk*32 + mf*16 + lr)*32 + lg*8);
-        const int ky = kk / 3, kx = kk - ky*3;
-        #pragma unroll
-        for (int nf = 0; nf < 3; ++nf) {
-            bf16x8 bv = *(const bf16x8*)&lds[((lg*6 + (w + ky))*48 + (nf*16 + lr + kx))*8];
-            #pragma unroll
-            for (int mf = 0; mf < 2; ++mf)
-                acc[mf][nf] = __builtin_amdgcn_mfma_f32_16x16x32_bf16(af[mf], bv, acc[mf][nf], 0, 0, 0);
-        }
-    }
-    const int y = r0 + w;
-    const int cb = lg*4;
-    {
-        float ls[2][4], lq[2][4], br[2][4];
-        #pragma unroll
-        for (int mf = 0; mf < 2; ++mf)
-            #pragma unroll
-            for (int i = 0; i < 4; ++i) {
-                ls[mf][i] = 0.f; lq[mf][i] = 0.f;
-                br[mf][i] = bs2[mf*16 + cb + i];
-            }
-        #pragma unroll
-        for (int nf = 0; nf < 3; ++nf) {
-            int x = nf*16 + lr;
-            bool xv = (x < 40);
-            #pragma unroll
-            for (int mf = 0; mf < 2; ++mf) {
-                u16x4 pk;
-                #pragma unroll
-                for (int i = 0; i < 4; ++i) {
-                    float v = acc[mf][nf][i] + br[mf][i];
-                    if (xv) { ls[mf][i] += v; lq[mf][i] = fmaf(v, v, lq[mf][i]); }
-                    pk[i] = f2bf(v);
-                }
-                if (xv) {
-                    int cg1 = mf*2 + (lg >> 1);
-                    *(u16x4*)(z2p + ((((size_t)b*4 + cg1)*46 + (y+2))*48 + (x+2))*8 + (lg&1)*4) = pk;
-                }
-            }
-        }
-        #pragma unroll
-        for (int mf = 0; mf < 2; ++mf)
-            #pragma unroll
-            for (int i = 0; i < 4; ++i) {
-                float s0 = ls[mf][i], q0 = lq[mf][i];
-                #pragma unroll
-                for (int m = 1; m < 16; m <<= 1) { s0 += __shfl_xor(s0, m, 64); q0 += __shfl_xor(q0, m, 64); }
-                if (lr == 0) { atomicAdd(&ssum[mf*16 + cb + i], s0); atomicAdd(&ssq[mf*16 + cb + i], q0); }
-            }
-    }
-    __syncthreads();
-    if (t < 32) { atomicAdd(&statsOut[t*2], ssum[t]); atomicAdd(&statsOut[t*2+1], ssq[t]); }
-}
-
-__global__ __launch_bounds__(256) void k_dconv1_mfma(const ushort* __restrict__ z2p,
-                                                     const ushort* __restrict__ apck,
-                                                     const float* __restrict__ bd1,
-                                                     const float* __restrict__ g2,
-                                                     const float* __restrict__ be2,
-                                                     const float* __restrict__ statsIn,
-                                                     ushort* __restrict__ z3p,
-                                                     float* __restrict__ statsOut) {
-    __shared__ ushort lds[4*6*48*8 + 32];
-    __shared__ float sc[32], sh[32], ssum[32], ssq[32];
-    const int rt = blockIdx.x, b = blockIdx.y, t = threadIdx.x;
-    const int w = t >> 6, lane = t & 63, lr = lane & 15, lg = lane >> 4;
-    const int r0 = rt * 4;
-    if (t < 32) {
-        bn_coef(statsIn, g2, be2, t, 1.f/25600.f, sc[t], sh[t]);
-        ssum[t] = 0.f; ssq[t] = 0.f;
-    }
-    __syncthreads();
-    f32x4 acc[2][3];
-    #pragma unroll
-    for (int mf = 0; mf < 2; ++mf)
-        #pragma unroll
-        for (int nf = 0; nf < 3; ++nf)
-            acc[mf][nf] = (f32x4){0.f, 0.f, 0.f, 0.f};
-
-    for (int u = t; u < 1152; u += 256) {
-        int cg = u / 288, rem = u - cg*288;
-        int rr = rem / 48, xx = rem - rr*48;
-        int row = r0 + rr;
-        uint4 v = {0u,0u,0u,0u};
-        if (row >= 2 && row <= 41 && xx >= 2 && xx <= 41) {
-            uint4 raw = *(const uint4*)(z2p + ((((size_t)b*4 + cg)*46 + row)*48 + xx)*8);
-            unsigned arr[4] = {raw.x, raw.y, raw.z, raw.w};
-            ushort h[8];
-            #pragma unroll
-            for (int e = 0; e < 8; ++e) {
-                ushort hv = (e & 1) ? (ushort)(arr[e>>1] >> 16) : (ushort)(arr[e>>1] & 0xffffu);
-                float f = fmaxf(fmaf(bf2f(hv), sc[cg*8 + e], sh[cg*8 + e]), 0.f);
-                h[e] = f2bf(f);
-            }
-            v.x = h[0] | ((unsigned)h[1] << 16);
-            v.y = h[2] | ((unsigned)h[3] << 16);
-            v.z = h[4] | ((unsigned)h[5] << 16);
-            v.w = h[6] | ((unsigned)h[7] << 16);
-        }
-        *(uint4*)(lds + (size_t)u*8) = v;
-    }
-    __syncthreads();
-    #pragma unroll
-    for (int kk = 0; kk < 9; ++kk) {
-        bf16x8 af[2];
-        #pragma unroll
-        for (int mf = 0; mf < 2; ++mf)
-            af[mf] = *(const bf16x8*)(apck + (size_t)(kk*32 + mf*16 + lr)*32 + lg*8);
-        const int ky = kk / 3, kx = kk - ky*3;
-        #pragma unroll
-        for (int nf = 0; nf < 3; ++nf) {
-            bf16x8 bv = *(const bf16x8*)&lds[((lg*6 + (w + ky))*48 + (nf*16 + lr + kx))*8];
-            #pragma unroll
-            for (int mf = 0; mf < 2; ++mf)
-                acc[mf][nf] = __builtin_amdgcn_mfma_f32_16x16x32_bf16(af[mf], bv, acc[mf][nf], 0, 0, 0);
-        }
-    }
-    const int y = r0 + w;
-    const int cb = lg*4;
-    if (y < 42) {
-        float ls[2][4], lq[2][4], br[2][4];
-        #pragma unroll
-        for (int mf = 0; mf < 2; ++mf)
-            #pragma unroll
-            for (int i = 0; i < 4; ++i) {
-                ls[mf][i] = 0.f; lq[mf][i] = 0.f;
-                br[mf][i] = bd1[mf*16 + cb + i];
-            }
-        #pragma unroll
-        for (int nf = 0; nf < 3; ++nf) {
-            int x = nf*16 + lr;
-            bool xv = (x < 42);
-            #pragma unroll
-            for (int mf = 0; mf < 2; ++mf) {
-                u16x4 pk;
-                #pragma unroll
-                for (int i = 0; i < 4; ++i) {
-                    float v = acc[mf][nf][i] + br[mf][i];
-                    if (xv) { ls[mf][i] += v; lq[mf][i] = fmaf(v, v, lq[mf][i]); }
-                    pk[i] = f2bf(v);
-                }
-                if (xv) {
-                    int cg1 = mf*2 + (lg >> 1);
-                    *(u16x4*)(z3p + ((((size_t)b*4 + cg1)*46 + (y+2))*48 + (x+2))*8 + (lg&1)*4) = pk;
-                }
-            }
-        }
-        #pragma unroll
-        for (int mf = 0; mf < 2; ++mf)
-            #pragma unroll
-            for (int i = 0; i < 4; ++i) {
-                float s0 = ls[mf][i], q0 = lq[mf][i];
-                #pragma unroll
-                for (int m = 1; m < 16; m <<= 1) { s0 += __shfl_xor(s0, m, 64); q0 += __shfl_xor(q0, m, 64); }
-                if (lr == 0) { atomicAdd(&ssum[mf*16 + cb + i], s0); atomicAdd(&ssq[mf*16 + cb + i], q0); }
-            }
-    }
-    __syncthreads();
-    if (t < 32) { atomicAdd(&statsOut[t*2], ssum[t]); atomicAdd(&statsOut[t*2+1], ssq[t]); }
-}
-
-__global__ __launch_bounds__(256) void k_dconv2(const ushort* __restrict__ z3p,
-                                                const float* __restrict__ wd2,
-                                                const float* __restrict__ bd2,
-                                                const float* __restrict__ g3,
-                                                const float* __restrict__ be3,
-                                                const float* __restrict__ stats,
-                                                float* __restrict__ satt) {
-    __shared__ float sc[32], sh[32], wf[32][9];
-    const int b = blockIdx.y, t = threadIdx.x;
-    if (t < 32) bn_coef(stats, g3, be3, t, 1.f/28224.f, sc[t], sh[t]);
-    for (int u = t; u < 288; u += 256) {
-        int c = u / 9, k = u - c*9;
-        wf[c][k] = wd2[c*9 + 8 - k];
-    }
-    __syncthreads();
-    const int pix = blockIdx.x * 256 + t;
-    if (pix >= P_) return;
-    const int y = pix / 44, x = pix - y*44;
-    float acc = bd2[0];
-    #pragma unroll
-    for (int kk = 0; kk < 9; ++kk) {
-        int ky = kk / 3, kx = kk - ky*3;
-        int ry = y + ky, rx = x + kx;
-        if (ry < 2 || ry > 43 || rx < 2 || rx > 43) continue;
-        #pragma unroll
-        for (int cg = 0; cg < 4; ++cg) {
-            uint4 raw = *(const uint4*)(z3p + ((((size_t)b*4 + cg)*46 + ry)*48 + rx)*8);
-            unsigned arr[4] = {raw.x, raw.y, raw.z, raw.w};
-            #pragma unroll
-            for (int e = 0; e < 8; ++e) {
-                ushort hv = (e & 1) ? (ushort)(arr[e>>1] >> 16) : (ushort)(arr[e>>1] & 0xffffu);
-                float f = fmaxf(fmaf(bf2f(hv), sc[cg*8 + e], sh[cg*8 + e]), 0.f);
-                acc = fmaf(f, wf[cg*8 + e][kk], acc);
-            }
-        }
-    }
-    satt[(size_t)b*P_ + pix] = 1.f / (1.f + expf(-acc));
 }
 
 extern "C" void kernel_launch(void* const* d_in, const int* in_sizes, int n_in,
@@ -689,10 +696,10 @@
     float* out = (float*)d_out;
     float* ws  = (float*)d_ws;
 
-    float* satt  = ws;
-    float* catt  = satt + 30976;
-    float* dcor  = catt + 1024;
-    float* stats = dcor + 1024;
+    float*    satt   = ws;
+    float*    catt   = satt + 30976;
+    float*    dcorp  = catt + 1024;
+    float*    stats  = dcorp + 4096;
     ushort* hcp    = (ushort*)(stats + 192);
     ushort* wpck   = hcp    + 2355200;
     ushort* apck2  = wpck   + 147456;
@@ -705,12 +712,13 @@
     ushort* z3p    = z2p    + 1130496;
     ushort* xpck   = z3p    + 1130496;
 
-    k_setup<<<2936, 256, 0, stream>>>(w_hc, w_hf, w_s2, w_d1, w_s1, rgb, depth,
-                                      wpck, apck2, apck3, apck1, xpck, depthb, dcor, stats);
-
-    k_hcconv<<<dim3(11,2,16), 256, 0, stream>>>(xpck, wpck, b_hc, hcp);
-    k_Umfma<<<dim3(19,16), 256, 0, stream>>>(apck1, depthb, upck,
-                                             dcor, w_l1, bl1, w_l2, bl2, catt);
+    k_setup<<<3320, 256, 0, stream>>>(w_hc, w_hf, w_s2, w_d1, w_s1, rgb, depth,
+                                      wpck, apck2, apck3, apck1, xpck, depthb,
+                                      dcorp, stats);
+
+    k_front<<<656, 256, 0, stream>>>(xpck, wpck, b_hc, hcp,
+                                     apck1, depthb, upck,
+                                     dcorp, w_l1, bl1, w_l2, bl2, catt);
 
     k_conv1_mfma<<<dim3(11,16), 256, 0, stream>>>(xpck, upck, bs1, z1p, stats);
     k_conv2_mfma<<<dim3(10,16), 256, 0, stream>>>(z1p, apck2, bs2, g1, be1, stats, z2p, stats + 64);
```

New measurement: 136.2 us, median of 2. 1.15x faster.
